# Optimization experiments

Measured on AMD Instinct MI355X. Metric: run time of the kernel, lower is better.

The kernel has to match this reference:

```python
import jax, jax.numpy as jnp
import numpy as np

HEADS = 16
TARGET_TOKENS = 128  # deterministic choice of image_tokens (original picks randomly from [729,128])


def _1d_sincos(embed_dim, pos):
    omega = np.arange(embed_dim // 2, dtype=np.float32)
    omega /= embed_dim / 2.0
    omega = 1.0 / 10000 ** omega
    out = np.einsum('m,d->md', pos.reshape(-1), omega)
    return np.concatenate([np.sin(out), np.cos(out)], axis=1)


def spatial_pos_embed(embed_dim, grid_size):
    d_sp = embed_dim // 4 * 3
    gh = np.arange(grid_size, dtype=np.float32)
    grid = np.stack(np.meshgrid(gh, gh), axis=0).reshape([2, 1, grid_size, grid_size])
    emb = np.concatenate([_1d_sincos(d_sp // 2, grid[0]), _1d_sincos(d_sp // 2, grid[1])], axis=1)
    emb = emb[np.newaxis]
    pad = np.zeros((1, emb.shape[1], embed_dim - d_sp), dtype=np.float32)
    return np.concatenate([pad, emb], axis=-1).reshape(1, grid_size * grid_size, embed_dim)


def setup_inputs() -> dict:
    key = jax.random.key(0)
    ks = jax.random.split(key, 4)
    B, P, C, H = 64, 729, 1152, 3584
    x = jax.random.normal(ks[0], (B, P, C), jnp.float32)
    w1 = jax.random.normal(ks[1], (C, H), jnp.float32) * (1.0 / np.sqrt(C))
    b1 = jnp.zeros((H,), jnp.float32)
    w2 = jax.random.normal(ks[2], (H, H), jnp.float32) * (1.0 / np.sqrt(H))
    b2 = jnp.zeros((H,), jnp.float32)
    spatial_pos = jnp.asarray(spatial_pos_embed(C, 27))
    return {'x': x, 'spatial_pos': spatial_pos, 'w1': w1, 'b1': b1,
            'w2': w2, 'b2': b2, 'local_num_frames': 1}


def _match_indices(metric, r):
    # ToMe bipartite soft matching: metric [B, T, d]
    metric = metric / jnp.linalg.norm(metric, axis=-1, keepdims=True)
    a, b = metric[:, ::2], metric[:, 1::2]
    scores = jnp.einsum('bic,bjc->bij', a, b)   # [B, Ta, Tb]
    node_max = scores.max(-1)
    node_idx = scores.argmax(-1)
    edge_idx = jnp.argsort(-node_max, axis=-1)
    unm_idx = edge_idx[:, r:]                    # kept src tokens
    src_idx = edge_idx[:, :r]                    # merged src tokens
    dst_idx = jnp.take_along_axis(node_idx, src_idx, axis=-1)
    return unm_idx, src_idx, dst_idx


def _merge_sum(x, unm_idx, src_idx, dst_idx):
    src, dst = x[:, ::2], x[:, 1::2]
    unm = jnp.take_along_axis(src, unm_idx[:, :, None], axis=1)
    sel = jnp.take_along_axis(src, src_idx[:, :, None], axis=1)
    dst = jax.vmap(lambda d, i, v: d.at[i].add(v))(dst, dst_idx, sel)
    return jnp.concatenate([unm, dst], axis=1)


def merge_tokens(x, target, heads):
    b, p, c = x.shape
    if p == target:
        return x
    rs, tmp = [], p
    while tmp != target:
        if tmp - target <= tmp // 2:
            rs.append(tmp - target)
            break
        rs.append(tmp // 2)
        tmp -= tmp // 2
    size = jnp.ones((b, p, 1), x.dtype)
    for r in rs:  # static schedule, e.g. [364, 182, 55]
        t = x.shape[1]
        metric = x.reshape(b, t, heads, c // heads).mean(2)
        idxs = _match_indices(metric, r)
        x = _merge_sum(x * size, *idxs)
        size = _merge_sum(size, *idxs)
        x = x / size
    return x


def reference(x, spatial_pos, w1, b1, w2, b2, local_num_frames):
    # is_image=True path
    x = x + spatial_pos
    x = merge_tokens(x, TARGET_TOKENS, HEADS)
    h = jax.nn.gelu(jnp.einsum('bpc,ch->bph', x, w1) + b1, approximate=False)
    return jnp.einsum('bph,ho->bpo', h, w2) + b2
```

## Files before the change

### kernel.cpp

```cpp
#include <hip/hip_runtime.h>
#include <hip/hip_bf16.h>
#include <stdint.h>

#define BB 64
#define P0 729
#define CC 1152
#define HD 72
#define NHEAD 16
#define HH 3584
#define TT 128
#define NSTR 365
#define SCB 384
#define MAXCB 6

typedef __hip_bfloat16 bf16;
typedef unsigned short u16;
typedef __attribute__((ext_vector_type(8))) short short8;
typedef __attribute__((ext_vector_type(4))) float floatx4;

__device__ inline u16 f2bf(float v) {
  bf16 h = __float2bfloat16(v);
  return *(u16*)&h;
}

__device__ inline void load_lds16(const void* g, void* l) {
  __builtin_amdgcn_global_load_lds(
      (const __attribute__((address_space(1))) uint32_t*)g,
      (__attribute__((address_space(3))) uint32_t*)l, 16, 0, 0);
}

__global__ __launch_bounds__(128)
void k_init(const float* __restrict__ x, const float* __restrict__ pos,
            double* __restrict__ mo, int* __restrict__ amap) {
  __shared__ float xs[CC], ps[CC];
  int bp = blockIdx.x;
  int p = bp % P0;
  int tid = threadIdx.x;
  const float4* xr = (const float4*)(x + (size_t)bp * CC);
  const float4* pr = (const float4*)(pos + (size_t)p * CC);
  for (int idx = tid; idx < CC / 4; idx += 128) {
    ((float4*)xs)[idx] = xr[idx];
    ((float4*)ps)[idx] = pr[idx];
  }
  __syncthreads();
  if (tid < HD) {
    double s = 0.0;
    #pragma unroll
    for (int h = 0; h < NHEAD; ++h) {
      int c = h * HD + tid;
      s += (double)xs[c] + (double)ps[c];
    }
    mo[(size_t)bp * HD + tid] = s * (1.0 / 16.0);
  }
  if (tid == 0) amap[bp] = p;
}

__global__ void k_rnorm(const double* __restrict__ m, double* __restrict__ rn, int t) {
  int bi = blockIdx.x;
  int lane = threadIdx.x;
  const double* row = m + (size_t)bi * HD;
  double v = 0.0;
  if (lane < HD) { double a = row[lane]; v = a * a; }
  if (lane < HD - 64) { double a = row[lane + 64]; v += a * a; }
  for (int off = 32; off; off >>= 1) v += __shfl_down(v, off, 64);
  if (lane == 0) {
    int b = bi / t, i = bi % t;
    rn[b * P0 + i] = 1.0 / sqrt(v);
  }
}

__global__ __launch_bounds__(256)
void k_score2(const double* __restrict__ m, const double* __restrict__ rn,
              double* __restrict__ pmax, int* __restrict__ pidx,
              int t, int s, int d) {
  __shared__ double sL[64][37];
  __shared__ double sD[64][37];
  int b = blockIdx.z;
  int i0 = blockIdx.x * 64, j0 = blockIdx.y * 64;
  int tid = threadIdx.x;
  int tx = tid & 15, ty = tid >> 4;
  double acc[4][4] = {};
  for (int kc = 0; kc < HD; kc += 36) {
    for (int idx = tid; idx < 64 * 36; idx += 256) {
      int row = idx / 36, k = idx - row * 36;
      int i = i0 + row;
      sL[row][k] = (i < s) ? m[((size_t)b * t + 2 * i) * HD + kc + k] : 0.0;
      int j = j0 + row;
      sD[row][k] = (j < d) ? m[((size_t)b * t + 2 * j + 1) * HD + kc + k] : 0.0;
    }
    __syncthreads();
    #pragma unroll 6
    for (int k = 0; k < 36; ++k) {
      double la[4], ld[4];
      #pragma unroll
      for (int a = 0; a < 4; ++a) la[a] = sL[ty + 16 * a][k];
      #pragma unroll
      for (int c = 0; c < 4; ++c) ld[c] = sD[tx + 16 * c][k];
      #pragma unroll
      for (int a = 0; a < 4; ++a)
        #pragma unroll
        for (int c = 0; c < 4; ++c)
          acc[a][c] += la[a] * ld[c];
    }
    __syncthreads();
  }
  #pragma unroll
  for (int a = 0; a < 4; ++a) {
    int i = i0 + ty + 16 * a;
    double rni = (i < s) ? rn[b * P0 + 2 * i] : 0.0;
    double best = -1e300; int bj = 0x7fffffff;
    #pragma unroll
    for (int c = 0; c < 4; ++c) {
      int j = j0 + tx + 16 * c;
      double sc = (j < d) ? acc[a][c] * rni * rn[b * P0 + 2 * j + 1] : -1e300;
      if (sc > best) { best = sc; bj = j; }
    }
    for (int off = 8; off; off >>= 1) {
      double ov = __shfl_down(best, off, 16);
      int oj = __shfl_down(bj, off, 16);
      if (ov > best || (ov == best && oj < bj)) { best = ov; bj = oj; }
    }
    if (tx == 0 && i < s) {
      pmax[((size_t)b * MAXCB + blockIdx.y) * SCB + i] = best;
      pidx[((size_t)b * MAXCB + blockIdx.y) * SCB + i] = bj;
    }
  }
}

__global__ void k_colred(const double* __restrict__ pmax, const int* __restrict__ pidx,
                         double* __restrict__ nmax, int* __restrict__ nidx,
                         int s, int ncb) {
  int b = blockIdx.x, i = threadIdx.x;
  if (i >= s) return;
  double best = -1e300; int bj = 0x7fffffff;
  for (int cb = 0; cb < ncb; ++cb) {
    double v = pmax[((size_t)b * MAXCB + cb) * SCB + i];
    int j = pidx[((size_t)b * MAXCB + cb) * SCB + i];
    if (v > best) { best = v; bj = j; }
  }
  nmax[b * NSTR + i] = best; nidx[b * NSTR + i] = bj;
}

template <int SZ>
__global__ __launch_bounds__(512)
void k_sort(const double* __restrict__ nmax, int* __restrict__ eidx, int s) {
  __shared__ double v[SZ];
  __shared__ int ix[SZ];
  int b = blockIdx.x, tid = threadIdx.x;
  if (tid < s) { v[tid] = nmax[b * NSTR + tid]; ix[tid] = tid; }
  else { v[tid] = -1e308; ix[tid] = 1024 + tid; }
  __syncthreads();
  for (int k = 2; k <= SZ; k <<= 1)
    for (int j = k >> 1; j > 0; j >>= 1) {
      int l = tid ^ j;
      if (l > tid) {
        double va = v[tid], vb = v[l]; int ia = ix[tid], ib = ix[l];
        bool b_before_a = (vb > va) || (vb == va && ib < ia);
        bool a_before_b = (va > vb) || (va == vb && ia < ib);
        bool dir = ((tid & k) == 0);
        bool sw = dir ? b_before_a : a_before_b;
        if (sw) { v[tid] = vb; v[l] = va; ix[tid] = ib; ix[l] = ia; }
      }
      __syncthreads();
    }
  if (tid < s) eidx[b * NSTR + tid] = ix[tid];
}

__global__ __launch_bounds__(512)
void k_mapround(const int* __restrict__ eidx, const int* __restrict__ nidx,
                int* __restrict__ amap, int t, int s, int r, int unm) {
  __shared__ int pos_of[NSTR];
  __shared__ int rmap[P0];
  int b = blockIdx.x, tid = threadIdx.x;
  for (int q = tid; q < s; q += 512) pos_of[eidx[b * NSTR + q]] = q;
  __syncthreads();
  for (int j = tid; j < t; j += 512) {
    int nm;
    if (j & 1) {
      nm = unm + (j >> 1);
    } else {
      int i = j >> 1;
      int q = pos_of[i];
      nm = (q >= r) ? (q - r)
                    : (unm + nidx[b * NSTR + i]);
    }
    rmap[j] = nm;
  }
  __syncthreads();
  for (int p = tid; p < P0; p += 512) {
    int cur = amap[b * P0 + p];
    amap[b * P0 + p] = rmap[cur];
  }
}

__global__ void k_gather_d(const double* __restrict__ mo, double* __restrict__ mn,
                           const int* __restrict__ eidx,
                           int t, int r, int unm, int tnew) {
  size_t idx = (size_t)blockIdx.x * 256 + threadIdx.x;
  size_t total = (size_t)BB * tnew * HD;
  if (idx >= total) return;
  int k = idx % HD;
  int o = (idx / HD) % tnew;
  int b = idx / ((size_t)HD * tnew);
  int tok = (o < unm) ? 2 * eidx[b * NSTR + r + o] : 2 * (o - unm) + 1;
  mn[idx] = mo[((size_t)b * t + tok) * HD + k];
}

__global__ void k_scatter_d(const double* __restrict__ mo, double* __restrict__ mn,
                            const int* __restrict__ eidx, const int* __restrict__ nidx,
                            int t, int r, int unm, int tnew) {
  size_t idx = (size_t)blockIdx.x * 256 + threadIdx.x;
  size_t total = (size_t)BB * r * HD;
  if (idx >= total) return;
  int k = idx % HD;
  int q = (idx / HD) % r;
  int b = idx / ((size_t)HD * r);
  int si = eidx[b * NSTR + q];
  int di = nidx[b * NSTR + si];
  atomicAdd(&mn[((size_t)b * tnew + unm + di) * HD + k],
            mo[((size_t)b * t + 2 * si) * HD + k]);
}

__global__ __launch_bounds__(256)
void k_buildcsr(const int* __restrict__ amap, int* __restrict__ sizes,
                int* __restrict__ offs, int* __restrict__ list) {
  __shared__ int cnt[TT], off_s[TT], cur[TT];
  int b = blockIdx.x, tid = threadIdx.x;
  if (tid < TT) { cnt[tid] = 0; cur[tid] = 0; }
  __syncthreads();
  for (int p = tid; p < P0; p += 256) atomicAdd(&cnt[amap[b * P0 + p]], 1);
  __syncthreads();
  if (tid == 0) {
    int acc = 0;
    for (int o = 0; o < TT; ++o) { off_s[o] = acc; acc += cnt[o]; }
  }
  __syncthreads();
  if (tid < TT) { sizes[b * TT + tid] = cnt[tid]; offs[b * TT + tid] = off_s[tid]; }
  for (int p = tid; p < P0; p += 256) {
    int o = amap[b * P0 + p];
    int pos = atomicAdd(&cur[o], 1);
    list[b * P0 + off_s[o] + pos] = p;
  }
}

__global__ __launch_bounds__(256)
void k_assemble(const float* __restrict__ x, const float* __restrict__ pos,
                const int* __restrict__ sizes, const int* __restrict__ offs,
                const int* __restrict__ list, bf16* __restrict__ xb) {
  int o = blockIdx.x, b = blockIdx.y, tid = threadIdx.x;
  int n = sizes[b * TT + o];
  int off = offs[b * TT + o];
  const int C4 = CC / 4;
  float4 a0 = {0.f, 0.f, 0.f, 0.f}, a1 = {0.f, 0.f, 0.f, 0.f};
  for (int i = 0; i < n; ++i) {
    int p = list[b * P0 + off + i];
    const float4* xr = (const float4*)(x + ((size_t)b * P0 + p) * CC);
    const float4* pr = (const float4*)(pos + (size_t)p * CC);
    float4 v = xr[tid], w = pr[tid];
    a0.x += v.x + w.x; a0.y += v.y + w.y; a0.z += v.z + w.z; a0.w += v.w + w.w;
    if (tid < C4 - 256) {
      float4 v1 = xr[tid + 256], w1 = pr[tid + 256];
      a1.x += v1.x + w1.x; a1.y += v1.y + w1.y; a1.z += v1.z + w1.z; a1.w += v1.w + w1.w;
    }
  }
  float inv = 1.0f / (float)n;
  bf16* orow = xb + ((size_t)b * TT + o) * CC;
  ushort4 pk;
  pk.x = f2bf(a0.x * inv);
  pk.y = f2bf(a0.y * inv);
  pk.z = f2bf(a0.z * inv);
  pk.w = f2bf(a0.w * inv);
  ((ushort4*)orow)[tid] = pk;
  if (tid < C4 - 256) {
    ushort4 pk1;
    pk1.x = f2bf(a1.x * inv);
    pk1.y = f2bf(a1.y * inv);
    pk1.z = f2bf(a1.z * inv);
    pk1.w = f2bf(a1.w * inv);
    ((ushort4*)orow)[tid + 256] = pk1;
  }
}

__global__ void k_transpose(const float* __restrict__ w, bf16* __restrict__ wt,
                            int K, int N) {
  __shared__ float tile[32][33];
  int n0 = blockIdx.x * 32, k0 = blockIdx.y * 32;
  int tx = threadIdx.x, ty = threadIdx.y;
  #pragma unroll
  for (int yy = 0; yy < 32; yy += 8)
    tile[ty + yy][tx] = w[(size_t)(k0 + ty + yy) * N + n0 + tx];
  __syncthreads();
  #pragma unroll
  for (int yy = 0; yy < 32; yy += 8)
    wt[(size_t)(n0 + ty + yy) * K + k0 + tx] = __float2bfloat16(tile[tx][ty + yy]);
}

template <int EPI>
__global__ __launch_bounds__(256)
void k_gemm(const u16* __restrict__ A, const u16* __restrict__ Bt,
            const float* __restrict__ bias, void* __restrict__ Cout,
            int M, int N, int K) {
  __shared__ u16 sA[128 * 32];
  __shared__ u16 sB[128 * 32];
  int tid = threadIdx.x;
  int m0 = blockIdx.y * 128, n0 = blockIdx.x * 128;
  int wave = tid >> 6, lane = tid & 63;
  int wm = (wave & 1) * 64, wn = (wave >> 1) * 64;
  int quad = lane >> 4, lrow = lane & 15;
  floatx4 acc[4][4] = {};
  const u16* gA = A + (size_t)(m0 + tid / 4) * K + (tid % 4) * 8;
  const u16* gB = Bt + (size_t)(n0 + tid / 4) * K + (tid % 4) * 8;
  for (int k0 = 0; k0 < K; k0 += 32) {
    load_lds16(gA + k0, &sA[tid * 8]);
    load_lds16(gA + (size_t)64 * K + k0, &sA[2048 + tid * 8]);
    load_lds16(gB + k0, &sB[tid * 8]);
    load_lds16(gB + (size_t)64 * K + k0, &sB[2048 + tid * 8]);
    __syncthreads();
    short8 af[4], bfr[4];
    #pragma unroll
    for (int mt = 0; mt < 4; ++mt)
      af[mt] = *(const short8*)&sA[(wm + mt * 16 + lrow) * 32 + quad * 8];
    #pragma unroll
    for (int nt = 0; nt < 4; ++nt)
      bfr[nt] = *(const short8*)&sB[(wn + nt * 16 + lrow) * 32 + quad * 8];
    #pragma unroll
    for (int mt = 0; mt < 4; ++mt)
      #pragma unroll
      for (int nt = 0; nt < 4; ++nt)
        acc[mt][nt] = __builtin_amdgcn_mfma_f32_16x16x32_bf16(af[mt], bfr[nt], acc[mt][nt], 0, 0, 0);
    __syncthreads();
  }
  #pragma unroll
  for (int mt = 0; mt < 4; ++mt)
    #pragma unroll
    for (int nt = 0; nt < 4; ++nt)
      #pragma unroll
      for (int rg = 0; rg < 4; ++rg) {
        int row = m0 + wm + mt * 16 + quad * 4 + rg;
        int col = n0 + wn + nt * 16 + lrow;
        float v = acc[mt][nt][rg] + bias[col];
        if (EPI == 0) {
          float g = 0.5f * v * (1.0f + erff(v * 0.70710678118654752f));
          ((bf16*)Cout)[(size_t)row * N + col] = __float2bfloat16(g);
        } else {
          ((float*)Cout)[(size_t)row * N + col] = v;
        }
      }
}

extern "C" void kernel_launch(void* const* d_in, const int* in_sizes, int n_in,
                              void* d_out, int out_size, void* d_ws, size_t ws_size,
                              hipStream_t stream) {
  const float* x   = (const float*)d_in[0];
  const float* pos = (const float*)d_in[1];
  const float* w1  = (const float*)d_in[2];
  const float* b1  = (const float*)d_in[3];
  const float* w2  = (const float*)d_in[4];
  const float* b2  = (const float*)d_in[5];

  uint8_t* wsp = (uint8_t*)d_ws;
  size_t off = 0;
  auto alloc = [&](size_t bytes) -> void* {
    void* p = wsp + off;
    off += (bytes + 255) & ~(size_t)255;
    return p;
  };
  double* m_a  = (double*)alloc((size_t)BB * P0 * HD * 8);
  double* m_b  = (double*)alloc((size_t)BB * NSTR * HD * 8);
  double* rn   = (double*)alloc((size_t)BB * P0 * 8);
  double* nmax = (double*)alloc((size_t)BB * NSTR * 8);
  int*    nidx = (int*)alloc((size_t)BB * NSTR * 4);
  int*    eidx = (int*)alloc((size_t)BB * NSTR * 4);
  double* pmax = (double*)alloc((size_t)BB * MAXCB * SCB * 8);
  int*    pidx = (int*)alloc((size_t)BB * MAXCB * SCB * 4);
  int*    amap = (int*)alloc((size_t)BB * P0 * 4);
  int*    szs  = (int*)alloc((size_t)BB * TT * 4);
  int*    offs = (int*)alloc((size_t)BB * TT * 4);
  int*    list = (int*)alloc((size_t)BB * P0 * 4);
  bf16*   xb   = (bf16*)alloc((size_t)BB * TT * CC * 2);
  bf16*   w1t  = (bf16*)alloc((size_t)HH * CC * 2);
  bf16*   w2t  = (bf16*)alloc((size_t)HH * HH * 2);
  bf16*   hb   = (bf16*)alloc((size_t)BB * TT * HH * 2);

  k_init<<<BB * P0, 128, 0, stream>>>(x, pos, m_a, amap);
  dim3 tb(32, 8);
  k_transpose<<<dim3(HH / 32, CC / 32), tb, 0, stream>>>(w1, w1t, CC, HH);
  k_transpose<<<dim3(HH / 32, HH / 32), tb, 0, stream>>>(w2, w2t, HH, HH);

  struct Rnd { int t, s, d, r, unm, tnew; };
  const Rnd R[3] = {{729, 365, 364, 364, 1, 365},
                    {365, 183, 182, 182, 1, 183},
                    {183,  92,  91,  55, 37, 128}};
  double* msrc[3] = {m_a, m_b, m_a};
  double* mdst[3] = {m_b, m_a, m_b};

  for (int rr = 0; rr < 3; ++rr) {
    Rnd q = R[rr];
    k_rnorm<<<BB * q.t, 64, 0, stream>>>(msrc[rr], rn, q.t);
    int rt = (q.s + 63) / 64, ct = (q.d + 63) / 64;
    dim3 sg(rt, ct, BB);
    k_score2<<<sg, 256, 0, stream>>>(msrc[rr], rn, pmax, pidx, q.t, q.s, q.d);
    k_colred<<<BB, 512, 0, stream>>>(pmax, pidx, nmax, nidx, q.s, ct);
    if (rr == 0)      k_sort<512><<<BB, 512, 0, stream>>>(nmax, eidx, q.s);
    else if (rr == 1) k_sort<256><<<BB, 256, 0, stream>>>(nmax, eidx, q.s);
    else              k_sort<128><<<BB, 128, 0, stream>>>(nmax, eidx, q.s);
    k_mapround<<<BB, 512, 0, stream>>>(eidx, nidx, amap, q.t, q.s, q.r, q.unm);
    if (rr < 2) {
      size_t tg = (size_t)BB * q.tnew * HD;
      k_gather_d<<<(tg + 255) / 256, 256, 0, stream>>>(msrc[rr], mdst[rr], eidx, q.t, q.r, q.unm, q.tnew);
      size_t ts = (size_t)BB * q.r * HD;
      k_scatter_d<<<(ts + 255) / 256, 256, 0, stream>>>(msrc[rr], mdst[rr], eidx, nidx, q.t, q.r, q.unm, q.tnew);
    }
  }

  k_buildcsr<<<BB, 256, 0, stream>>>(amap, szs, offs, list);
  k_assemble<<<dim3(TT, BB), 256, 0, stream>>>(x, pos, szs, offs, list, xb);

  k_gemm<0><<<dim3(HH / 128, (BB * TT) / 128), 256, 0, stream>>>(
      (const u16*)xb, (const u16*)w1t, b1, hb, BB * TT, HH, CC);
  k_gemm<1><<<dim3(HH / 128, (BB * TT) / 128), 256, 0, stream>>>(
      (const u16*)hb, (const u16*)w2t, b2, d_out, BB * TT, HH, HH);
}
```

Baseline: 1.334 ms.

## Rewrite GEMM as 256x256 tile, 8-wave, double-buffered pipelined MFMA kernel

```diff
diff --git a/kernel.cpp b/kernel.cpp
--- a/kernel.cpp
+++ b/kernel.cpp
@@ -295,57 +295,155 @@
     wt[(size_t)(n0 + ty + yy) * K + k0 + tx] = __float2bfloat16(tile[tx][ty + yy]);
 }
 
+
+#define SBAR __builtin_amdgcn_sched_barrier(0)
+
+#define STAGE_A(BUF, HHF, KT) do {                                        \
+    int ktc_ = (KT) < nkt ? (KT) : nkt - 1;                               \
+    const u16* s_ = gA + (size_t)(HHF) * 128 * K + ktc_ * 64;             \
+    u16* d_ = dA + (BUF) * 16384 + (HHF) * 8192;                          \
+    load_lds16(s_, d_);                                                   \
+    load_lds16(s_ + (size_t)64 * K, d_ + 4096);                           \
+  } while (0)
+
+#define STAGE_B(BUF, HHF, KT) do {                                        \
+    int ktc_ = (KT) < nkt ? (KT) : nkt - 1;                               \
+    const u16* s_ = gB + (size_t)(HHF) * 128 * K + ktc_ * 64;             \
+    u16* d_ = dB + (BUF) * 16384 + (HHF) * 8192;                          \
+    load_lds16(s_, d_);                                                   \
+    load_lds16(s_ + (size_t)64 * K, d_ + 4096);                           \
+  } while (0)
+
+#define LOADA(QA) do {                                                    \
+    _Pragma("unroll")                                                     \
+    for (int f_ = 0; f_ < 4; ++f_) {                                      \
+      const u16* p_ = Ab + ((QA) * 128 + wr64 + f_ * 16 + lrow) * 64;     \
+      af[f_][0] = *(const short8*)(p_ + swo0);                            \
+      af[f_][1] = *(const short8*)(p_ + swo1);                            \
+    }                                                                     \
+  } while (0)
+
+#define LOADB(QB) do {                                                    \
+    _Pragma("unroll")                                                     \
+    for (int g_ = 0; g_ < 2; ++g_) {                                      \
+      const u16* p_ = Bb + ((QB) * 128 + wc32 + g_ * 16 + lrow) * 64;     \
+      bfr[g_][0] = *(const short8*)(p_ + swo0);                           \
+      bfr[g_][1] = *(const short8*)(p_ + swo1);                           \
+    }                                                                     \
+  } while (0)
+
+#define DO_MFMA(QA, QB) do {                                              \
+    _Pragma("unroll")                                                     \
+    for (int ks_ = 0; ks_ < 2; ++ks_)                                     \
+      _Pragma("unroll")                                                   \
+      for (int f_ = 0; f_ < 4; ++f_)                                      \
+        _Pragma("unroll")                                                 \
+        for (int g_ = 0; g_ < 2; ++g_)                                    \
+          acc[QA][QB][f_][g_] = __builtin_amdgcn_mfma_f32_16x16x32_bf16(  \
+              af[f_][ks_], bfr[g_][ks_], acc[QA][QB][f_][g_], 0, 0, 0);   \
+  } while (0)
+
+#define MIDBAR() do {                                                     \
+    SBAR;                                                                 \
+    __builtin_amdgcn_s_barrier();                                         \
+    asm volatile("s_waitcnt lgkmcnt(0)" ::: "memory");                    \
+    SBAR;                                                                 \
+    __builtin_amdgcn_s_setprio(1);                                        \
+  } while (0)
+
+#define ENDBAR() do {                                                     \
+    __builtin_amdgcn_s_setprio(0);                                        \
+    SBAR;                                                                 \
+    __builtin_amdgcn_s_barrier();                                         \
+    SBAR;                                                                 \
+  } while (0)
+
+#define ENDBAR_VM() do {                                                  \
+    __builtin_amdgcn_s_setprio(0);                                        \
+    SBAR;                                                                 \
+    asm volatile("s_waitcnt vmcnt(6)" ::: "memory");                      \
+    SBAR;                                                                 \
+    __builtin_amdgcn_s_barrier();                                         \
+    SBAR;                                                                 \
+  } while (0)
+
 template <int EPI>
-__global__ __launch_bounds__(256)
+__global__ __launch_bounds__(512, 2)
 void k_gemm(const u16* __restrict__ A, const u16* __restrict__ Bt,
             const float* __restrict__ bias, void* __restrict__ Cout,
             int M, int N, int K) {
-  __shared__ u16 sA[128 * 32];
-  __shared__ u16 sB[128 * 32];
-  int tid = threadIdx.x;
-  int m0 = blockIdx.y * 128, n0 = blockIdx.x * 128;
-  int wave = tid >> 6, lane = tid & 63;
-  int wm = (wave & 1) * 64, wn = (wave >> 1) * 64;
-  int quad = lane >> 4, lrow = lane & 15;
-  floatx4 acc[4][4] = {};
-  const u16* gA = A + (size_t)(m0 + tid / 4) * K + (tid % 4) * 8;
-  const u16* gB = Bt + (size_t)(n0 + tid / 4) * K + (tid % 4) * 8;
-  for (int k0 = 0; k0 < K; k0 += 32) {
-    load_lds16(gA + k0, &sA[tid * 8]);
-    load_lds16(gA + (size_t)64 * K + k0, &sA[2048 + tid * 8]);
-    load_lds16(gB + k0, &sB[tid * 8]);
-    load_lds16(gB + (size_t)64 * K + k0, &sB[2048 + tid * 8]);
-    __syncthreads();
-    short8 af[4], bfr[4];
+  __shared__ u16 sAall[32768];
+  __shared__ u16 sBall[32768];
+  (void)M;
+  const int tid = threadIdx.x;
+  const int m0 = blockIdx.y * 256, n0 = blockIdx.x * 256;
+  const int wave = tid >> 6, lane = tid & 63;
+  const int wr64 = (wave >> 2) * 64;
+  const int wc32 = (wave & 3) * 32;
+  const int quad = lane >> 4, lrow = lane & 15;
+  const int sw = lrow & 7;
+  const int swo0 = ((quad ^ sw)) << 3;
+  const int swo1 = (((quad | 4) ^ sw)) << 3;
+  const int nkt = K >> 6;
+
+  const int r = tid >> 3;
+  const int c16 = (tid & 7) ^ (r & 7);
+  const u16* gA = A + (size_t)(m0 + r) * K + c16 * 8;
+  const u16* gB = Bt + (size_t)(n0 + r) * K + c16 * 8;
+  u16* dA = sAall + (tid << 3);
+  u16* dB = sBall + (tid << 3);
+
+  floatx4 acc[2][2][4][2] = {};
+  short8 af[4][2], bfr[2][2];
+
+  STAGE_A(0, 0, 0); STAGE_B(0, 1, 0); STAGE_A(0, 1, 0); STAGE_B(0, 0, 0);
+  STAGE_A(1, 0, 1); STAGE_B(1, 1, 1); STAGE_A(1, 1, 1);
+  SBAR;
+  asm volatile("s_waitcnt vmcnt(6)" ::: "memory");
+  SBAR;
+  __builtin_amdgcn_s_barrier();
+  SBAR;
+
+  for (int t = 0; t < nkt; ++t) {
+    const int bb = t & 1;
+    const u16* Ab = sAall + bb * 16384;
+    const u16* Bb = sBall + bb * 16384;
+    LOADA(0); LOADB(0);
+    STAGE_B(bb ^ 1, 0, t + 1);
+    MIDBAR(); DO_MFMA(0, 0); ENDBAR();
+    LOADB(1);
+    STAGE_A(bb, 0, t + 2);
+    MIDBAR(); DO_MFMA(0, 1); ENDBAR();
+    LOADA(1);
+    STAGE_B(bb, 1, t + 2);
+    MIDBAR(); DO_MFMA(1, 1); ENDBAR();
+    LOADB(0);
+    STAGE_A(bb, 1, t + 2);
+    MIDBAR(); DO_MFMA(1, 0); ENDBAR_VM();
+  }
+
+  #pragma unroll
+  for (int qb = 0; qb < 2; ++qb)
     #pragma unroll
-    for (int mt = 0; mt < 4; ++mt)
-      af[mt] = *(const short8*)&sA[(wm + mt * 16 + lrow) * 32 + quad * 8];
-    #pragma unroll
-    for (int nt = 0; nt < 4; ++nt)
-      bfr[nt] = *(const short8*)&sB[(wn + nt * 16 + lrow) * 32 + quad * 8];
-    #pragma unroll
-    for (int mt = 0; mt < 4; ++mt)
+    for (int g = 0; g < 2; ++g) {
+      int col = n0 + qb * 128 + wc32 + g * 16 + lrow;
+      float bc = bias[col];
       #pragma unroll
-      for (int nt = 0; nt < 4; ++nt)
-        acc[mt][nt] = __builtin_amdgcn_mfma_f32_16x16x32_bf16(af[mt], bfr[nt], acc[mt][nt], 0, 0, 0);
-    __syncthreads();
-  }
-  #pragma unroll
-  for (int mt = 0; mt < 4; ++mt)
-    #pragma unroll
-    for (int nt = 0; nt < 4; ++nt)
-      #pragma unroll
-      for (int rg = 0; rg < 4; ++rg) {
-        int row = m0 + wm + mt * 16 + quad * 4 + rg;
-        int col = n0 + wn + nt * 16 + lrow;
-        float v = acc[mt][nt][rg] + bias[col];
-        if (EPI == 0) {
-          float g = 0.5f * v * (1.0f + erff(v * 0.70710678118654752f));
-          ((bf16*)Cout)[(size_t)row * N + col] = __float2bfloat16(g);
-        } else {
-          ((float*)Cout)[(size_t)row * N + col] = v;
-        }
-      }
+      for (int qa = 0; qa < 2; ++qa)
+        #pragma unroll
+        for (int f = 0; f < 4; ++f)
+          #pragma unroll
+          for (int rg = 0; rg < 4; ++rg) {
+            int row = m0 + qa * 128 + wr64 + f * 16 + quad * 4 + rg;
+            float v = acc[qa][qb][f][g][rg] + bc;
+            if (EPI == 0) {
+              float gl = 0.5f * v * (1.0f + erff(v * 0.70710678118654752f));
+              ((bf16*)Cout)[(size_t)row * N + col] = __float2bfloat16(gl);
+            } else {
+              ((float*)Cout)[(size_t)row * N + col] = v;
+            }
+          }
+    }
 }
 
 extern "C" void kernel_launch(void* const* d_in, const int* in_sizes, int n_in,
@@ -416,8 +514,8 @@
   k_buildcsr<<<BB, 256, 0, stream>>>(amap, szs, offs, list);
   k_assemble<<<dim3(TT, BB), 256, 0, stream>>>(x, pos, szs, offs, list, xb);
 
-  k_gemm<0><<<dim3(HH / 128, (BB * TT) / 128), 256, 0, stream>>>(
+  k_gemm<0><<<dim3(HH / 256, (BB * TT) / 256), 512, 0, stream>>>(
       (const u16*)xb, (const u16*)w1t, b1, hb, BB * TT, HH, CC);
-  k_gemm<1><<<dim3(HH / 128, (BB * TT) / 128), 256, 0, stream>>>(
+  k_gemm<1><<<dim3(HH / 256, (BB * TT) / 256), 512, 0, stream>>>(
       (const u16*)hb, (const u16*)w2t, b2, d_out, BB * TT, HH, HH);
 }
```

After: 1.404 ms. +5.3%, slower.
